# Kernel optimization log

Measured on AMD Instinct MI355X. Metric: run time of the kernel, lower is better.

The kernel has to match this reference:

```python
import jax, jax.numpy as jnp
import numpy as np

N_LAYERS = 4
D = 768
H = 12
DK = D // H
FF = 2048
SD = 5
DIM_LOC = 6
EPS = 1e-10


def layer_norm(x, g, b, eps=1e-5):
    m = x.mean(-1, keepdims=True)
    v = ((x - m) ** 2).mean(-1, keepdims=True)
    return (x - m) / jnp.sqrt(v + eps) * g + b


def calc_pairwise_locs(centers):
    # centers: [b, l, 3] -> [b, l, t, 5] spatial relation features ('center' type, dist-normalized)
    rel = centers[:, :, None, :] - centers[:, None, :, :]
    d = jnp.sqrt(jnp.sum(rel ** 2, -1) + EPS)
    max_d = jnp.max(d.reshape(d.shape[0], -1), -1)
    dn = d / max_d[:, None, None]
    d2 = jnp.sqrt(jnp.sum(rel[..., :2] ** 2, -1) + EPS)
    return jnp.stack([dn, rel[..., 2] / d, d2 / d, rel[..., 1] / d2, rel[..., 0] / d2], -1)


def setup_inputs() -> dict:
    key = jax.random.key(0)
    ks = jax.random.split(key, 32)
    B, L = 16, 512
    std = 0.02
    inp = {
        'obj_embeds': jax.random.normal(ks[0], (B, L, D), jnp.float32),
        'obj_locs': jax.random.uniform(ks[1], (B, L, DIM_LOC), jnp.float32) * 5.0,
        'obj_masks': jnp.ones((B, L), jnp.bool_),
        # single loc layer (obj_loc_encoding='same_all')
        'loc_w': jax.random.normal(ks[2], (DIM_LOC, D), jnp.float32) * std,
        'loc_b': jnp.zeros((D,), jnp.float32),
        'loc_ln_g': jnp.ones((D,), jnp.float32),
        'loc_ln_b': jnp.zeros((D,), jnp.float32),
        # per-layer params, stacked on leading layer dim
        'Wq': jax.random.normal(ks[3], (N_LAYERS, D, D), jnp.float32) * std,
        'bq': jnp.zeros((N_LAYERS, D), jnp.float32),
        'Wk': jax.random.normal(ks[4], (N_LAYERS, D, D), jnp.float32) * std,
        'bk': jnp.zeros((N_LAYERS, D), jnp.float32),
        'Wv': jax.random.normal(ks[5], (N_LAYERS, D, D), jnp.float32) * std,
        'bv': jnp.zeros((N_LAYERS, D), jnp.float32),
        'Wfc': jax.random.normal(ks[6], (N_LAYERS, D, D), jnp.float32) * std,
        'bfc': jnp.zeros((N_LAYERS, D), jnp.float32),
        'loc_fc_w': jax.random.normal(ks[7], (N_LAYERS, SD, H), jnp.float32) * std,
        'loc_fc_b': jnp.zeros((N_LAYERS, H), jnp.float32),
        'ln0_g': jnp.ones((N_LAYERS, D), jnp.float32),
        'ln0_b': jnp.zeros((N_LAYERS, D), jnp.float32),
        'W1': jax.random.normal(ks[8], (N_LAYERS, D, FF), jnp.float32) * std,
        'b1': jnp.zeros((N_LAYERS, FF), jnp.float32),
        'W2': jax.random.normal(ks[9], (N_LAYERS, FF, D), jnp.float32) * std,
        'b2': jnp.zeros((N_LAYERS, D), jnp.float32),
        'ln1_g': jnp.ones((N_LAYERS, D), jnp.float32),
        'ln1_b': jnp.zeros((N_LAYERS, D), jnp.float32),
        'ln2_g': jnp.ones((N_LAYERS, D), jnp.float32),
        'ln2_b': jnp.zeros((N_LAYERS, D), jnp.float32),
    }
    return inp


def _forward(obj_embeds, obj_locs, obj_masks, loc_w, loc_b, loc_ln_g, loc_ln_b,
             Wq, bq, Wk, bk, Wv, bv, Wfc, bfc, loc_fc_w, loc_fc_b, ln0_g, ln0_b,
             W1, b1, W2, b2, ln1_g, ln1_b, ln2_g, ln2_b):
    B, L, _ = obj_embeds.shape
    pl = calc_pairwise_locs(obj_locs[..., :3])        # [b,l,t,5]
    kpm = jnp.logical_not(obj_masks)                  # key_padding_mask: True = pad
    mask = kpm[:, None, None, :]                      # [b,1,1,t]
    query_pos = layer_norm(obj_locs @ loc_w + loc_b, loc_ln_g, loc_ln_b)
    x = obj_embeds
    scale = np.float32(1.0 / np.sqrt(DK))
    for i in range(N_LAYERS):
        x = x + query_pos  # obj_loc_encoding='same_all': add loc embedding every layer
        res = x
        q = (x @ Wq[i] + bq[i]).reshape(B, L, H, DK)
        k = (x @ Wk[i] + bk[i]).reshape(B, L, H, DK)
        v = (x @ Wv[i] + bv[i]).reshape(B, L, H, DK)
        attn = jnp.einsum('blhk,bthk->bhlt', q, k) * scale
        loc_attn = jax.nn.relu(jnp.einsum('bltd,dh->bhlt', pl, loc_fc_w[i])
                               + loc_fc_b[i][None, :, None, None])
        attn = jnp.where(mask, -1e30, attn)
        loc_attn = jnp.where(mask, 0.0, loc_attn)
        fused = jax.nn.softmax(jnp.log(jnp.clip(loc_attn, 1e-6)) + attn, axis=-1)
        out = jnp.einsum('bhlt,bthv->blhv', fused, v).reshape(B, L, D)
        out = out @ Wfc[i] + bfc[i]
        x2 = layer_norm(out + res, ln0_g[i], ln0_b[i])   # attn-internal residual + LN
        x = layer_norm(x + x2, ln1_g[i], ln1_b[i])       # encoder-layer norm1
        ff = jax.nn.gelu(x @ W1[i] + b1[i], approximate=False) @ W2[i] + b2[i]
        x = layer_norm(x + ff, ln2_g[i], ln2_b[i])       # encoder-layer norm2
    return x


def reference(obj_embeds, obj_locs, obj_masks, loc_w, loc_b, loc_ln_g, loc_ln_b,
              Wq, bq, Wk, bk, Wv, bv, Wfc, bfc, loc_fc_w, loc_fc_b, ln0_g, ln0_b,
              W1, b1, W2, b2, ln1_g, ln1_b, ln2_g, ln2_b):
    return _forward(obj_embeds, obj_locs, obj_masks, loc_w, loc_b, loc_ln_g, loc_ln_b,
                    Wq, bq, Wk, bk, Wv, bv, Wfc, bfc, loc_fc_w, loc_fc_b, ln0_g, ln0_b,
                    W1, b1, W2, b2, ln1_g, ln1_b, ln2_g, ln2_b)
```

## Files before the change

### kernel.cpp

```cpp
#include <hip/hip_runtime.h>
#include <hip/hip_bf16.h>
#include <math.h>

#define NL 4
#define D 768
#define H 12
#define DK 64
#define FF 2048
#define SD 5
#define DLOC 6
#define B 16
#define L 512
#define M (B*L)

typedef unsigned short u16;
typedef unsigned int u32;
typedef __attribute__((ext_vector_type(8))) __bf16 bf16x8;
typedef __attribute__((ext_vector_type(4))) float f32x4;

__device__ inline float b2f(u16 u){ u32 v = ((u32)u)<<16; return __builtin_bit_cast(float, v); }
__device__ inline u16 f2b(float f){ __hip_bfloat16 h = __float2bfloat16(f); return __builtin_bit_cast(u16, h); }

__device__ inline void gld16(const u16* g, u16* l) {
    __builtin_amdgcn_global_load_lds(
        (const __attribute__((address_space(1))) u32*)(const void*)g,
        (__attribute__((address_space(3))) u32*)(void*)l, 16, 0, 0);
}

__global__ __launch_bounds__(256) void maxd_kernel(const float* __restrict__ locs,
                                                   u32* __restrict__ maxd) {
    int b = blockIdx.x >> 5;
    int seg = blockIdx.x & 31;
    __shared__ float cx[L], cy[L], cz[L];
    for (int i = threadIdx.x; i < L; i += 256) {
        const float* p = locs + ((size_t)b*L + i)*DLOC;
        cx[i] = p[0]; cy[i] = p[1]; cz[i] = p[2];
    }
    __syncthreads();
    float mx = 0.f;
    int r0 = seg*16;
    #pragma unroll
    for (int r = 0; r < 16; ++r) {
        float px = cx[r0+r], py = cy[r0+r], pz = cz[r0+r];
        for (int c = threadIdx.x; c < L; c += 256) {
            float dx = px-cx[c], dy = py-cy[c], dz = pz-cz[c];
            mx = fmaxf(mx, dx*dx + dy*dy + dz*dz);
        }
    }
    #pragma unroll
    for (int m=1;m<64;m<<=1) mx = fmaxf(mx, __shfl_xor(mx, m));
    __shared__ float wred[4];
    if ((threadIdx.x & 63) == 0) wred[threadIdx.x >> 6] = mx;
    __syncthreads();
    if (threadIdx.x == 0) {
        float v = fmaxf(fmaxf(wred[0],wred[1]), fmaxf(wred[2],wred[3]));
        float d = sqrtf(v + 1e-10f);
        atomicMax(maxd + b, __builtin_bit_cast(u32, d));
    }
}

__global__ __launch_bounds__(256) void initq_kernel(const float* __restrict__ embeds,
    const float* __restrict__ locs, const float* __restrict__ lw, const float* __restrict__ lb,
    const float* __restrict__ lg, const float* __restrict__ lbb,
    float* __restrict__ x, u16* __restrict__ xb) {
    int row = blockIdx.x;
    float lc[DLOC];
    #pragma unroll
    for (int d=0; d<DLOC; d++) lc[d] = locs[(size_t)row*DLOC + d];
    float mv[3], s1 = 0.f, s2 = 0.f;
    #pragma unroll
    for (int e = 0; e < 3; e++) {
        int col = threadIdx.x + 256*e;
        float v = lb[col];
        #pragma unroll
        for (int d = 0; d < DLOC; d++) v += lc[d]*lw[d*D + col];
        mv[e] = v; s1 += v; s2 += v*v;
    }
    __shared__ float r1[256], r2[256];
    r1[threadIdx.x]=s1; r2[threadIdx.x]=s2; __syncthreads();
    for (int s=128;s>0;s>>=1){
        if(threadIdx.x<s){r1[threadIdx.x]+=r1[threadIdx.x+s]; r2[threadIdx.x]+=r2[threadIdx.x+s];}
        __syncthreads();
    }
    float mean = r1[0]*(1.0f/D);
    float var  = r2[0]*(1.0f/D) - mean*mean;
    float rstd = rsqrtf(var + 1e-5f);
    #pragma unroll
    for (int e=0;e<3;e++){
        int col = threadIdx.x+256*e;
        float qp = (mv[e]-mean)*rstd*lg[col]+lbb[col];
        float v = embeds[(size_t)row*D+col] + qp;
        x[(size_t)row*D+col] = v;
        xb[(size_t)row*D+col] = f2b(v);
    }
}

__global__ __launch_bounds__(256) void ln01_kernel(const float* __restrict__ t0f,
    const float* __restrict__ xin,
    const float* __restrict__ g0, const float* __restrict__ b0,
    const float* __restrict__ g1, const float* __restrict__ b1,
    float* __restrict__ xout, u16* __restrict__ xb) {
    int row = blockIdx.x;
    __shared__ float r1[256], r2[256];
    float xv[3], vv[3], s1=0.f, s2=0.f;
    #pragma unroll
    for (int e=0;e<3;e++){
        int col = threadIdx.x+256*e;
        float xr = xin[(size_t)row*D+col];
        float v = t0f[(size_t)row*D+col] + xr;
        xv[e]=xr; vv[e]=v; s1+=v; s2+=v*v;
    }
    r1[threadIdx.x]=s1; r2[threadIdx.x]=s2; __syncthreads();
    for (int s=128;s>0;s>>=1){
        if(threadIdx.x<s){r1[threadIdx.x]+=r1[threadIdx.x+s]; r2[threadIdx.x]+=r2[threadIdx.x+s];}
        __syncthreads();
    }
    float mean0 = r1[0]*(1.0f/D);
    float var0  = r2[0]*(1.0f/D) - mean0*mean0;
    float rstd0 = rsqrtf(var0 + 1e-5f);
    __syncthreads();
    float uv[3]; s1=0.f; s2=0.f;
    #pragma unroll
    for (int e=0;e<3;e++){
        int col = threadIdx.x+256*e;
        float x2 = (vv[e]-mean0)*rstd0*g0[col]+b0[col];
        float u = xv[e] + x2;
        uv[e]=u; s1+=u; s2+=u*u;
    }
    r1[threadIdx.x]=s1; r2[threadIdx.x]=s2; __syncthreads();
    for (int s=128;s>0;s>>=1){
        if(threadIdx.x<s){r1[threadIdx.x]+=r1[threadIdx.x+s]; r2[threadIdx.x]+=r2[threadIdx.x+s];}
        __syncthreads();
    }
    float mean1 = r1[0]*(1.0f/D);
    float var1  = r2[0]*(1.0f/D) - mean1*mean1;
    float rstd1 = rsqrtf(var1 + 1e-5f);
    #pragma unroll
    for (int e=0;e<3;e++){
        int col = threadIdx.x+256*e;
        float v = (uv[e]-mean1)*rstd1*g1[col]+b1[col];
        xout[(size_t)row*D+col] = v;
        xb[(size_t)row*D+col] = f2b(v);
    }
}

template<int LAST>
__global__ __launch_bounds__(256) void ln2q_kernel(const float* __restrict__ xin,
    const float* __restrict__ t0f, const float* __restrict__ g2, const float* __restrict__ b2,
    const float* __restrict__ locs, const float* __restrict__ lw, const float* __restrict__ lb,
    const float* __restrict__ lg, const float* __restrict__ lbb,
    float* __restrict__ xout, u16* __restrict__ xb) {
    int row = blockIdx.x;
    __shared__ float r1[256], r2[256], r3[256], r4[256];
    float lc[DLOC];
    if (!LAST) {
        #pragma unroll
        for (int d=0; d<DLOC; d++) lc[d] = locs[(size_t)row*DLOC + d];
    }
    float vv[3], mv[3], s1=0.f, s2=0.f, s3=0.f, s4=0.f;
    #pragma unroll
    for (int e=0;e<3;e++){
        int col = threadIdx.x+256*e;
        float v = xin[(size_t)row*D+col] + t0f[(size_t)row*D+col];
        vv[e]=v; s1+=v; s2+=v*v;
        if (!LAST) {
            float mvv = lb[col];
            #pragma unroll
            for (int d = 0; d < DLOC; d++) mvv += lc[d]*lw[d*D + col];
            mv[e]=mvv; s3+=mvv; s4+=mvv*mvv;
        }
    }
    r1[threadIdx.x]=s1; r2[threadIdx.x]=s2;
    if (!LAST) { r3[threadIdx.x]=s3; r4[threadIdx.x]=s4; }
    __syncthreads();
    for (int s=128;s>0;s>>=1){
        if(threadIdx.x<s){
            r1[threadIdx.x]+=r1[threadIdx.x+s]; r2[threadIdx.x]+=r2[threadIdx.x+s];
            if (!LAST){ r3[threadIdx.x]+=r3[threadIdx.x+s]; r4[threadIdx.x]+=r4[threadIdx.x+s]; }
        }
        __syncthreads();
    }
    float mean = r1[0]*(1.0f/D);
    float var  = r2[0]*(1.0f/D) - mean*mean;
    float rstd = rsqrtf(var + 1e-5f);
    float mean3=0.f, rstd3=0.f;
    if (!LAST) {
        mean3 = r3[0]*(1.0f/D);
        float var3 = r4[0]*(1.0f/D) - mean3*mean3;
        rstd3 = rsqrtf(var3 + 1e-5f);
    }
    #pragma unroll
    for (int e=0;e<3;e++){
        int col = threadIdx.x+256*e;
        float xn = (vv[e]-mean)*rstd*g2[col]+b2[col];
        if (LAST) {
            xout[(size_t)row*D+col] = xn;
        } else {
            float qp = (mv[e]-mean3)*rstd3*lg[col]+lbb[col];
            float v = xn + qp;
            xout[(size_t)row*D+col] = v;
            xb[(size_t)row*D+col] = f2b(v);
        }
    }
}

__global__ __launch_bounds__(256) void convT6_kernel(
    const float* __restrict__ Wq, const float* __restrict__ Wk,
    const float* __restrict__ Wv, const float* __restrict__ Wfc,
    const float* __restrict__ W1, const float* __restrict__ W2,
    u16* __restrict__ wq_t, u16* __restrict__ wfc_t,
    u16* __restrict__ w1_t, u16* __restrict__ w2_t) {
    int bid = blockIdx.x;
    const float* in; u16* outp; int K, N, nb, kb;
    if (bid < 1728) {
        int m = bid / 576, r = bid % 576;
        in = (m==0) ? Wq : (m==1) ? Wk : Wv;
        outp = wq_t + m*D*D; K = D; N = D; nb = r % 24; kb = r / 24;
    } else if (bid < 2304) {
        int r = bid - 1728;
        in = Wfc; outp = wfc_t; K = D; N = D; nb = r % 24; kb = r / 24;
    } else if (bid < 3840) {
        int r = bid - 2304;
        in = W1; outp = w1_t; K = D; N = FF; nb = r % 64; kb = r / 64;
    } else {
        int r = bid - 3840;
        in = W2; outp = w2_t; K = FF; N = D; nb = r % 24; kb = r / 24;
    }
    __shared__ float tile[32][33];
    int kbb = kb*32, nbb = nb*32;
    int tx = threadIdx.x & 31, ty = threadIdx.x >> 5;
    #pragma unroll
    for (int i=0;i<32;i+=8)
        tile[ty+i][tx] = in[(size_t)(kbb+ty+i)*N + nbb+tx];
    __syncthreads();
    #pragma unroll
    for (int i=0;i<32;i+=8)
        outp[(size_t)(nbb+ty+i)*K + kbb+tx] = f2b(tile[tx][ty+i]);
}

__global__ __launch_bounds__(256) void biaspack_kernel(const float* __restrict__ bq,
    const float* __restrict__ bk, const float* __restrict__ bv, float* __restrict__ outb) {
    int i = blockIdx.x*256 + threadIdx.x;
    int l = i / (3*D), j = i % (3*D);
    float v = (j < D) ? bq[l*D + j] : (j < 2*D ? bk[l*D + j - D] : bv[l*D + j - 2*D]);
    outb[i] = v;
}

template<int OUT_BF16, int ACT>
__global__ __launch_bounds__(256) void mm_kernel(
    const u16* __restrict__ A, const u16* __restrict__ Bt,
    const float* __restrict__ bias, void* __restrict__ Cout, int K, int N)
{
    __shared__ u16 As[2][128*32];
    __shared__ u16 Bs[2][128*32];
    const int tid = threadIdx.x;
    const int lane = tid & 63, wv = tid >> 6;
    const int m0 = blockIdx.y*128, n0 = blockIdx.x*128;
    const int wm = (wv>>1)*64, wn = (wv&1)*64;

    const u16* ag = A  + (size_t)(m0 + wv*16 + (lane>>2))*K + (lane&3)*8;
    const u16* bg = Bt + (size_t)(n0 + wv*16 + (lane>>2))*K + (lane&3)*8;
    const size_t rstep = (size_t)64*K;
    const int lofs = wv*512;

    f32x4 acc[4][4];
    #pragma unroll
    for (int i=0;i<4;i++)
        #pragma unroll
        for (int j=0;j<4;j++) acc[i][j] = (f32x4){0.f,0.f,0.f,0.f};

    const int lr = lane & 15, kq = lane >> 4;

    gld16(ag, &As[0][lofs]);
    gld16(ag + rstep, &As[0][2048+lofs]);
    gld16(bg, &Bs[0][lofs]);
    gld16(bg + rstep, &Bs[0][2048+lofs]);
    __syncthreads();

    int cur = 0;
    for (int k0 = 0; k0 < K; k0 += 32) {
        if (k0 + 32 < K) {
            int nx = cur ^ 1, kn = k0 + 32;
            gld16(ag + kn, &As[nx][lofs]);
            gld16(ag + rstep + kn, &As[nx][2048+lofs]);
            gld16(bg + kn, &Bs[nx][lofs]);
            gld16(bg + rstep + kn, &Bs[nx][2048+lofs]);
        }
        const u16* Arow = &As[cur][(wm + lr)*32 + kq*8];
        const u16* Brow = &Bs[cur][(wn + lr)*32 + kq*8];
        bf16x8 af[4], bfr[4];
        #pragma unroll
        for (int i=0;i<4;i++) af[i]  = *(const bf16x8*)(Arow + i*512);
        #pragma unroll
        for (int j=0;j<4;j++) bfr[j] = *(const bf16x8*)(Brow + j*512);
        #pragma unroll
        for (int i=0;i<4;i++)
            #pragma unroll
            for (int j=0;j<4;j++)
                acc[i][j] = __builtin_amdgcn_mfma_f32_16x16x32_bf16(af[i], bfr[j], acc[i][j], 0,0,0);
        __syncthreads();
        cur ^= 1;
    }

    const int cr = (lane>>4)*4, cc = lane & 15;
    #pragma unroll
    for (int i=0;i<4;i++) {
        int row = m0 + wm + i*16 + cr;
        #pragma unroll
        for (int j=0;j<4;j++) {
            int col = n0 + wn + j*16 + cc;
            float bv_ = bias[col];
            #pragma unroll
            for (int r=0;r<4;r++) {
                float v = acc[i][j][r] + bv_;
                if (ACT) v = 0.5f*v*(1.0f + erff(v*0.70710678f));
                if (OUT_BF16) ((u16*)Cout)[(size_t)(row+r)*N + col] = f2b(v);
                else        ((float*)Cout)[(size_t)(row+r)*N + col] = v;
            }
        }
    }
}

__global__ __launch_bounds__(256) void attn_kernel(
    const u16* __restrict__ qkv, const float* __restrict__ locs,
    const float* __restrict__ maxdp, const float* __restrict__ lfw,
    const float* __restrict__ lfb, u16* __restrict__ out)
{
    const int RS = 3*D;
    const float SC = 0.18033688f;
    const int bid = blockIdx.x;
    const int qt = bid & 7;
    const int hp = (bid >> 3) % 6;
    const int b  = bid / 48;
    const int qb = qt*64;
    const int h0 = hp*2;

    __shared__ u16 Ks[2][64*64];
    __shared__ u16 Vt[2][64*64];
    __shared__ u16 Pl[2][4*16*64];
    __shared__ float Cts[64][4];

    const int t = threadIdx.x;
    const int lane = t & 63, wv = t >> 6;
    const int l15 = lane & 15, l4 = lane >> 4;

    bf16x8 qf[2][2];
    {
        const u16* qr = qkv + (size_t)(b*L + qb + wv*16 + l15)*RS + h0*DK + l4*8;
        qf[0][0] = *(const bf16x8*)(qr);
        qf[0][1] = *(const bf16x8*)(qr + 32);
        qf[1][0] = *(const bf16x8*)(qr + DK);
        qf[1][1] = *(const bf16x8*)(qr + DK + 32);
    }
    float cqx[4], cqy[4], cqz[4];
    #pragma unroll
    for (int r=0;r<4;r++){
        const float* p = locs + (size_t)(b*L + qb + wv*16 + l4*4 + r)*DLOC;
        cqx[r]=p[0]; cqy[r]=p[1]; cqz[r]=p[2];
    }
    const float invmd = 1.0f / maxdp[b];
    float w0p[2], w1[2], w2[2], w3[2], w4[2], wbb[2];
    #pragma unroll
    for (int hh=0; hh<2; hh++){
        int h = h0+hh;
        w0p[hh] = lfw[0*H+h]*invmd; w1[hh]=lfw[1*H+h]; w2[hh]=lfw[2*H+h];
        w3[hh]=lfw[3*H+h]; w4[hh]=lfw[4*H+h]; wbb[hh]=lfb[h];
    }

    f32x4 oacc[2][4];
    float mrun[2][4], lrun[2][4];
    #pragma unroll
    for (int hh=0;hh<2;hh++)
        #pragma unroll
        for (int j=0;j<4;j++){ oacc[hh][j] = (f32x4){0.f,0.f,0.f,0.f};
                               mrun[hh][j] = -1e30f; lrun[hh][j] = 0.f; }

    const int r0s = (wv*64 + lane) >> 3;
    const int sslot = lane & 7;

    bf16x8 kreg[4];
    bf16x8 vreg[2][2];
    float ctr0=0.f, ctr1=0.f, ctr2=0.f;

    {
        const u16* kgb = qkv + (size_t)(b*L + 0)*RS + D + h0*DK;
        kreg[0] = *(const bf16x8*)(kgb + (size_t)r0s*RS + sslot*8);
        kreg[1] = *(const bf16x8*)(kgb + (size_t)(r0s+32)*RS + sslot*8);
        kreg[2] = *(const bf16x8*)(kgb + DK + (size_t)r0s*RS + sslot*8);
        kreg[3] = *(const bf16x8*)(kgb + DK + (size_t)(r0s+32)*RS + sslot*8);
        const u16* vp = qkv + (size_t)(b*L + 0 + lane)*RS + 2*D + h0*DK + wv*16;
        vreg[0][0] = *(const bf16x8*)(vp);
        vreg[0][1] = *(const bf16x8*)(vp + 8);
        vreg[1][0] = *(const bf16x8*)(vp + DK);
        vreg[1][1] = *(const bf16x8*)(vp + DK + 8);
        if (t < 64) {
            const float* p = locs + (size_t)(b*L + 0 + t)*DLOC;
            ctr0=p[0]; ctr1=p[1]; ctr2=p[2];
        }
    }

    for (int kt = 0; kt < L; kt += 64) {
        {
            int c0 = (sslot ^ (r0s & 7))*8;
            *(bf16x8*)(&Ks[0][r0s*64 + c0]) = kreg[0];
            *(bf16x8*)(&Ks[0][(r0s+32)*64 + c0]) = kreg[1];
            *(bf16x8*)(&Ks[1][r0s*64 + c0]) = kreg[2];
            *(bf16x8*)(&Ks[1][(r0s+32)*64 + c0]) = kreg[3];
            int d0 = wv*16;
            #pragma unroll
            for (int hh=0; hh<2; hh++)
                #pragma unroll
                for (int e=0;e<8;e++){
                    Vt[hh][(d0+e)*64   + (lane ^ (e<<3))] = ((const u16*)&vreg[hh][0])[e];
                    Vt[hh][(d0+8+e)*64 + (lane ^ (e<<3))] = ((const u16*)&vreg[hh][1])[e];
                }
            if (t < 64) { Cts[t][0]=ctr0; Cts[t][1]=ctr1; Cts[t][2]=ctr2; }
        }
        __syncthreads();

        if (kt + 64 < L) {
            const u16* kgb = qkv + (size_t)(b*L + kt + 64)*RS + D + h0*DK;
            kreg[0] = *(const bf16x8*)(kgb + (size_t)r0s*RS + sslot*8);
            kreg[1] = *(const bf16x8*)(kgb + (size_t)(r0s+32)*RS + sslot*8);
            kreg[2] = *(const bf16x8*)(kgb + DK + (size_t)r0s*RS + sslot*8);
            kreg[3] = *(const bf16x8*)(kgb + DK + (size_t)(r0s+32)*RS + sslot*8);
            const u16* vp = qkv + (size_t)(b*L + kt + 64 + lane)*RS + 2*D + h0*DK + wv*16;
            vreg[0][0] = *(const bf16x8*)(vp);
            vreg[0][1] = *(const bf16x8*)(vp + 8);
            vreg[1][0] = *(const bf16x8*)(vp + DK);
            vreg[1][1] = *(const bf16x8*)(vp + DK + 8);
            if (t < 64) {
                const float* p = locs + (size_t)(b*L + kt + 64 + t)*DLOC;
                ctr0=p[0]; ctr1=p[1]; ctr2=p[2];
            }
        }

        f32x4 sacc[2][4];
        #pragma unroll
        for (int hh=0;hh<2;hh++)
            #pragma unroll
            for (int j=0;j<4;j++){
                sacc[hh][j] = (f32x4){0.f,0.f,0.f,0.f};
                #pragma unroll
                for (int c=0;c<2;c++){
                    int row = j*16 + l15;
                    int slot = l4 + 4*c;
                    bf16x8 kf = *(const bf16x8*)(&Ks[hh][row*64 + ((slot ^ (row&7))*8)]);
                    sacc[hh][j] = __builtin_amdgcn_mfma_f32_16x16x32_bf16(qf[hh][c], kf, sacc[hh][j], 0,0,0);
                }
            }

        float ctx[4], cty[4], ctz[4];
        #pragma unroll
        for (int j=0;j<4;j++){
            int c = l15 + 16*j;
            ctx[j]=Cts[c][0]; cty[j]=Cts[c][1]; ctz[j]=Cts[c][2];
        }

        float alr[2][4];
        #pragma unroll
        for (int r=0;r<4;r++){
            float f0[4], f1[4], f2[4], f3[4], f4[4];
            #pragma unroll
            for (int j=0;j<4;j++){
                float rx = cqx[r]-ctx[j], ry = cqy[r]-cty[j], rz = cqz[r]-ctz[j];
                float d2e = fmaf(ry,ry, fmaf(rx,rx, 1e-10f));
                float r2  = fmaf(rz,rz, d2e);
                float invd  = __builtin_amdgcn_rsqf(r2);
                float invd2 = __builtin_amdgcn_rsqf(d2e);
                f0[j] = r2*invd;
                f1[j] = rz*invd;
                f2[j] = (d2e*invd2)*invd;
                f3[j] = ry*invd2;
                f4[j] = rx*invd2;
            }
            #pragma unroll
            for (int hh=0; hh<2; hh++){
                float sv[4], la[4];
                #pragma unroll
                for (int j=0;j<4;j++){
                    float z = fmaf(f0[j], w0p[hh],
                              fmaf(f1[j], w1[hh],
                              fmaf(f2[j], w2[hh],
                              fmaf(f3[j], w3[hh],
                              fmaf(f4[j], w4[hh], wbb[hh])))));
                    la[j] = fmaxf(z, 1e-6f);
                    sv[j] = sacc[hh][j][r]*SC;
                }
                float mx = fmaxf(fmaxf(sv[0],sv[1]), fmaxf(sv[2],sv[3]));
                #pragma unroll
                for (int msk=1; msk<16; msk<<=1) mx = fmaxf(mx, __shfl_xor(mx, msk));
                float mo = mrun[hh][r];
                float mn = fmaxf(mo, mx);
                float al = __builtin_amdgcn_exp2f(mo - mn);
                float sp = 0.f;
                u16* pw = &Pl[hh][wv*1024];
                int q = l4*4 + r, sw = (q&7)<<3;
                #pragma unroll
                for (int j=0;j<4;j++){
                    float p = la[j] * __builtin_amdgcn_exp2f(sv[j] - mn);
                    sp += p;
                    pw[q*64 + ((l15 + 16*j) ^ sw)] = f2b(p);
                }
                #pragma unroll
                for (int msk=1; msk<16; msk<<=1) sp += __shfl_xor(sp, msk);
                mrun[hh][r] = mn;
                lrun[hh][r] = lrun[hh][r]*al + sp;
                alr[hh][r] = al;
            }
        }

        #pragma unroll
        for (int hh=0; hh<2; hh++){
            #pragma unroll
            for (int j=0;j<4;j++)
                #pragma unroll
                for (int r=0;r<4;r++) oacc[hh][j][r] *= alr[hh][r];
            const u16* pr = &Pl[hh][wv*1024];
            #pragma unroll
            for (int c=0;c<2;c++){
                int prow = l15;
                int pslot = l4 + 4*c;
                bf16x8 pf = *(const bf16x8*)(pr + prow*64 + ((pslot ^ (prow&7))*8));
                #pragma unroll
                for (int j=0;j<4;j++){
                    int vrow = j*16 + l15;
                    int vslot = l4 + 4*c;
                    bf16x8 vf = *(const bf16x8*)(&Vt[hh][vrow*64 + ((vslot ^ (vrow&7))*8)]);
                    oacc[hh][j] = __builtin_amdgcn_mfma_f32_16x16x32_bf16(pf, vf, oacc[hh][j], 0,0,0);
                }
            }
        }
        __syncthreads();
    }

    #pragma unroll
    for (int hh=0; hh<2; hh++)
        #pragma unroll
        for (int r=0;r<4;r++){
            float inv = __builtin_amdgcn_rcpf(lrun[hh][r]);
            size_t obase = (size_t)(b*L + qb + wv*16 + l4*4 + r)*D + (h0+hh)*DK;
            #pragma unroll
            for (int j=0;j<4;j++)
                out[obase + l15 + 16*j] = f2b(oacc[hh][j][r] * inv);
        }
}

extern "C" void kernel_launch(void* const* d_in, const int* in_sizes, int n_in,
                              void* d_out, int out_size, void* d_ws, size_t ws_size,
                              hipStream_t stream) {
    const float* obj_embeds = (const float*)d_in[0];
    const float* obj_locs   = (const float*)d_in[1];
    const float* loc_w   = (const float*)d_in[3];
    const float* loc_b   = (const float*)d_in[4];
    const float* loc_ln_g= (const float*)d_in[5];
    const float* loc_ln_b= (const float*)d_in[6];
    const float* Wq = (const float*)d_in[7];
    const float* bq = (const float*)d_in[8];
    const float* Wk = (const float*)d_in[9];
    const float* bk = (const float*)d_in[10];
    const float* Wv = (const float*)d_in[11];
    const float* bv = (const float*)d_in[12];
    const float* Wfc= (const float*)d_in[13];
    const float* bfc= (const float*)d_in[14];
    const float* lfw= (const float*)d_in[15];
    const float* lfb= (const float*)d_in[16];
    const float* ln0_g = (const float*)d_in[17];
    const float* ln0_b = (const float*)d_in[18];
    const float* W1 = (const float*)d_in[19];
    const float* b1 = (const float*)d_in[20];
    const float* W2 = (const float*)d_in[21];
    const float* b2 = (const float*)d_in[22];
    const float* ln1_g = (const float*)d_in[23];
    const float* ln1_b = (const float*)d_in[24];
    const float* ln2_g = (const float*)d_in[25];
    const float* ln2_b = (const float*)d_in[26];

    float* x  = (float*)d_out;
    char* base = (char*)d_ws;
    u16*   xb    = (u16*)  (base);
    u16*   qkv   = (u16*)  (base + 12582912);
    u16*   aob   = (u16*)  (base + 50331648);
    float* t0f   = (float*)(base + 62914560);
    u16*   wq_t  = (u16*)  (base + 88080384);
    u16*   wfc_t = (u16*)  (base + 91619328);
    u16*   w1_t  = (u16*)  (base + 92798976);
    u16*   w2_t  = (u16*)  (base + 95944704);
    float* bqkv  = (float*)(base + 99090432);
    u32*   maxd  = (u32*)  (base + 99127296);
    u16*   h1b   = qkv;

    hipMemsetAsync(maxd, 0, B*sizeof(u32), stream);
    maxd_kernel<<<B*32, 256, 0, stream>>>(obj_locs, maxd);
    biaspack_kernel<<<(NL*3*D)/256, 256, 0, stream>>>(bq, bk, bv, bqkv);
    initq_kernel<<<M, 256, 0, stream>>>(obj_embeds, obj_locs, loc_w, loc_b,
                                        loc_ln_g, loc_ln_b, x, xb);

    for (int i = 0; i < NL; i++) {
        const size_t wo = (size_t)i*D*D;
        convT6_kernel<<<5376, 256, 0, stream>>>(Wq + wo, Wk + wo, Wv + wo, Wfc + wo,
                                                W1 + (size_t)i*D*FF, W2 + (size_t)i*FF*D,
                                                wq_t, wfc_t, w1_t, w2_t);

        mm_kernel<1,0><<<dim3(18,64), 256, 0, stream>>>(xb, wq_t, bqkv + i*3*D, qkv, D, 3*D);
        attn_kernel<<<B*6*8, 256, 0, stream>>>(qkv, obj_locs, (const float*)maxd,
                                               lfw + i*SD*H, lfb + i*H, aob);
        mm_kernel<0,0><<<dim3(6,64), 256, 0, stream>>>(aob, wfc_t, bfc + i*D, t0f, D, D);
        ln01_kernel<<<M, 256, 0, stream>>>(t0f, x, ln0_g + i*D, ln0_b + i*D,
                                           ln1_g + i*D, ln1_b + i*D, x, xb);
        mm_kernel<1,1><<<dim3(16,64), 256, 0, stream>>>(xb, w1_t, b1 + i*FF, h1b, D, FF);
        mm_kernel<0,0><<<dim3(6,64), 256, 0, stream>>>(h1b, w2_t, b2 + i*D, t0f, FF, D);
        if (i < NL-1)
            ln2q_kernel<0><<<M, 256, 0, stream>>>(x, t0f, ln2_g + i*D, ln2_b + i*D,
                obj_locs, loc_w, loc_b, loc_ln_g, loc_ln_b, x, xb);
        else
            ln2q_kernel<1><<<M, 256, 0, stream>>>(x, t0f, ln2_g + i*D, ln2_b + i*D,
                obj_locs, loc_w, loc_b, loc_ln_g, loc_ln_b, x, xb);
    }
}
```

Measured before the change: 1.353 ms.

## Cut attention kernel registers and LDS to raise occupancy

The attention kernel now targets four blocks per SIMD through launch bounds. It shrinks LDS by letting the P tile share the K buffer after an extra barrier. K tiles are loaded straight into LDS with global_load_lds rather than staged through registers, and Q is reloaded each iteration instead of kept live. Register prefetching of the next K/V tile is dropped, so latency hiding relies on having more resident waves, at the cost of an extra sync per tile and repeated Q loads.

```diff
diff --git a/kernel.cpp b/kernel.cpp
--- a/kernel.cpp
+++ b/kernel.cpp
@@ -321,7 +321,7 @@
     }
 }
 
-__global__ __launch_bounds__(256) void attn_kernel(
+__global__ __launch_bounds__(256, 4) void attn_kernel(
     const u16* __restrict__ qkv, const float* __restrict__ locs,
     const float* __restrict__ maxdp, const float* __restrict__ lfw,
     const float* __restrict__ lfb, u16* __restrict__ out)
@@ -335,23 +335,14 @@
     const int qb = qt*64;
     const int h0 = hp*2;
 
-    __shared__ u16 Ks[2][64*64];
-    __shared__ u16 Vt[2][64*64];
-    __shared__ u16 Pl[2][4*16*64];
+    __shared__ u16 KP[2][4096];
+    __shared__ u16 Vt[2][4096];
     __shared__ float Cts[64][4];
 
     const int t = threadIdx.x;
     const int lane = t & 63, wv = t >> 6;
     const int l15 = lane & 15, l4 = lane >> 4;
 
-    bf16x8 qf[2][2];
-    {
-        const u16* qr = qkv + (size_t)(b*L + qb + wv*16 + l15)*RS + h0*DK + l4*8;
-        qf[0][0] = *(const bf16x8*)(qr);
-        qf[0][1] = *(const bf16x8*)(qr + 32);
-        qf[1][0] = *(const bf16x8*)(qr + DK);
-        qf[1][1] = *(const bf16x8*)(qr + DK + 32);
-    }
     float cqx[4], cqy[4], cqz[4];
     #pragma unroll
     for (int r=0;r<4;r++){
@@ -376,90 +367,66 @@
                                mrun[hh][j] = -1e30f; lrun[hh][j] = 0.f; }
 
     const int r0s = (wv*64 + lane) >> 3;
-    const int sslot = lane & 7;
-
-    bf16x8 kreg[4];
-    bf16x8 vreg[2][2];
-    float ctr0=0.f, ctr1=0.f, ctr2=0.f;
-
-    {
-        const u16* kgb = qkv + (size_t)(b*L + 0)*RS + D + h0*DK;
-        kreg[0] = *(const bf16x8*)(kgb + (size_t)r0s*RS + sslot*8);
-        kreg[1] = *(const bf16x8*)(kgb + (size_t)(r0s+32)*RS + sslot*8);
-        kreg[2] = *(const bf16x8*)(kgb + DK + (size_t)r0s*RS + sslot*8);
-        kreg[3] = *(const bf16x8*)(kgb + DK + (size_t)(r0s+32)*RS + sslot*8);
-        const u16* vp = qkv + (size_t)(b*L + 0 + lane)*RS + 2*D + h0*DK + wv*16;
-        vreg[0][0] = *(const bf16x8*)(vp);
-        vreg[0][1] = *(const bf16x8*)(vp + 8);
-        vreg[1][0] = *(const bf16x8*)(vp + DK);
-        vreg[1][1] = *(const bf16x8*)(vp + DK + 8);
+    const int c0 = ((lane & 7) ^ (r0s & 7))*8;
+    const u16* qr = qkv + (size_t)(b*L + qb + wv*16 + l15)*RS + h0*DK + l4*8;
+
+    for (int kt = 0; kt < L; kt += 64) {
+        const u16* kgb = qkv + (size_t)(b*L + kt)*RS + D + h0*DK;
+        gld16(kgb + (size_t)r0s*RS + c0,           &KP[0][wv*512]);
+        gld16(kgb + (size_t)(r0s+32)*RS + c0,      &KP[0][2048 + wv*512]);
+        gld16(kgb + DK + (size_t)r0s*RS + c0,      &KP[1][wv*512]);
+        gld16(kgb + DK + (size_t)(r0s+32)*RS + c0, &KP[1][2048 + wv*512]);
+        const u16* vp = qkv + (size_t)(b*L + kt + lane)*RS + 2*D + h0*DK + wv*16;
+        bf16x8 v0a = *(const bf16x8*)(vp);
+        bf16x8 v0b = *(const bf16x8*)(vp + 8);
+        bf16x8 v1a = *(const bf16x8*)(vp + DK);
+        bf16x8 v1b = *(const bf16x8*)(vp + DK + 8);
+        bf16x8 qf00 = *(const bf16x8*)(qr);
+        bf16x8 qf01 = *(const bf16x8*)(qr + 32);
+        bf16x8 qf10 = *(const bf16x8*)(qr + DK);
+        bf16x8 qf11 = *(const bf16x8*)(qr + DK + 32);
         if (t < 64) {
-            const float* p = locs + (size_t)(b*L + 0 + t)*DLOC;
-            ctr0=p[0]; ctr1=p[1]; ctr2=p[2];
-        }
-    }
-
-    for (int kt = 0; kt < L; kt += 64) {
+            const float* p = locs + (size_t)(b*L + kt + t)*DLOC;
+            Cts[t][0]=p[0]; Cts[t][1]=p[1]; Cts[t][2]=p[2];
+        }
+        __syncthreads();
+
         {
-            int c0 = (sslot ^ (r0s & 7))*8;
-            *(bf16x8*)(&Ks[0][r0s*64 + c0]) = kreg[0];
-            *(bf16x8*)(&Ks[0][(r0s+32)*64 + c0]) = kreg[1];
-            *(bf16x8*)(&Ks[1][r0s*64 + c0]) = kreg[2];
-            *(bf16x8*)(&Ks[1][(r0s+32)*64 + c0]) = kreg[3];
             int d0 = wv*16;
             #pragma unroll
-            for (int hh=0; hh<2; hh++)
-                #pragma unroll
-                for (int e=0;e<8;e++){
-                    Vt[hh][(d0+e)*64   + (lane ^ (e<<3))] = ((const u16*)&vreg[hh][0])[e];
-                    Vt[hh][(d0+8+e)*64 + (lane ^ (e<<3))] = ((const u16*)&vreg[hh][1])[e];
-                }
-            if (t < 64) { Cts[t][0]=ctr0; Cts[t][1]=ctr1; Cts[t][2]=ctr2; }
-        }
-        __syncthreads();
-
-        if (kt + 64 < L) {
-            const u16* kgb = qkv + (size_t)(b*L + kt + 64)*RS + D + h0*DK;
-            kreg[0] = *(const bf16x8*)(kgb + (size_t)r0s*RS + sslot*8);
-            kreg[1] = *(const bf16x8*)(kgb + (size_t)(r0s+32)*RS + sslot*8);
-            kreg[2] = *(const bf16x8*)(kgb + DK + (size_t)r0s*RS + sslot*8);
-            kreg[3] = *(const bf16x8*)(kgb + DK + (size_t)(r0s+32)*RS + sslot*8);
-            const u16* vp = qkv + (size_t)(b*L + kt + 64 + lane)*RS + 2*D + h0*DK + wv*16;
-            vreg[0][0] = *(const bf16x8*)(vp);
-            vreg[0][1] = *(const bf16x8*)(vp + 8);
-            vreg[1][0] = *(const bf16x8*)(vp + DK);
-            vreg[1][1] = *(const bf16x8*)(vp + DK + 8);
-            if (t < 64) {
-                const float* p = locs + (size_t)(b*L + kt + 64 + t)*DLOC;
-                ctr0=p[0]; ctr1=p[1]; ctr2=p[2];
-            }
-        }
-
+            for (int e=0;e<8;e++){
+                int csw = lane ^ (e<<3);
+                Vt[0][(d0+e)*64   + csw] = ((const u16*)&v0a)[e];
+                Vt[0][(d0+8+e)*64 + csw] = ((const u16*)&v0b)[e];
+                Vt[1][(d0+e)*64   + csw] = ((const u16*)&v1a)[e];
+                Vt[1][(d0+8+e)*64 + csw] = ((const u16*)&v1b)[e];
+            }
+        }
         f32x4 sacc[2][4];
         #pragma unroll
-        for (int hh=0;hh<2;hh++)
+        for (int j=0;j<4;j++){
+            int row = j*16 + l15;
+            sacc[0][j] = (f32x4){0.f,0.f,0.f,0.f};
+            sacc[1][j] = (f32x4){0.f,0.f,0.f,0.f};
+            #pragma unroll
+            for (int c=0;c<2;c++){
+                int ofs = row*64 + (((l4 + 4*c) ^ (row&7))*8);
+                bf16x8 kf0 = *(const bf16x8*)(&KP[0][ofs]);
+                bf16x8 kf1 = *(const bf16x8*)(&KP[1][ofs]);
+                sacc[0][j] = __builtin_amdgcn_mfma_f32_16x16x32_bf16(c?qf01:qf00, kf0, sacc[0][j], 0,0,0);
+                sacc[1][j] = __builtin_amdgcn_mfma_f32_16x16x32_bf16(c?qf11:qf10, kf1, sacc[1][j], 0,0,0);
+            }
+        }
+        __syncthreads();
+
+        #pragma unroll
+        for (int r=0;r<4;r++){
+            float ctx[4], cty[4], ctz[4];
             #pragma unroll
             for (int j=0;j<4;j++){
-                sacc[hh][j] = (f32x4){0.f,0.f,0.f,0.f};
-                #pragma unroll
-                for (int c=0;c<2;c++){
-                    int row = j*16 + l15;
-                    int slot = l4 + 4*c;
-                    bf16x8 kf = *(const bf16x8*)(&Ks[hh][row*64 + ((slot ^ (row&7))*8)]);
-                    sacc[hh][j] = __builtin_amdgcn_mfma_f32_16x16x32_bf16(qf[hh][c], kf, sacc[hh][j], 0,0,0);
-                }
-            }
-
-        float ctx[4], cty[4], ctz[4];
-        #pragma unroll
-        for (int j=0;j<4;j++){
-            int c = l15 + 16*j;
-            ctx[j]=Cts[c][0]; cty[j]=Cts[c][1]; ctz[j]=Cts[c][2];
-        }
-
-        float alr[2][4];
-        #pragma unroll
-        for (int r=0;r<4;r++){
+                int c = l15 + 16*j;
+                ctx[j]=Cts[c][0]; cty[j]=Cts[c][1]; ctz[j]=Cts[c][2];
+            }
             float f0[4], f1[4], f2[4], f3[4], f4[4];
             #pragma unroll
             for (int j=0;j<4;j++){
@@ -494,7 +461,7 @@
                 float mn = fmaxf(mo, mx);
                 float al = __builtin_amdgcn_exp2f(mo - mn);
                 float sp = 0.f;
-                u16* pw = &Pl[hh][wv*1024];
+                u16* pw = &KP[hh][wv*1024];
                 int q = l4*4 + r, sw = (q&7)<<3;
                 #pragma unroll
                 for (int j=0;j<4;j++){
@@ -506,27 +473,22 @@
                 for (int msk=1; msk<16; msk<<=1) sp += __shfl_xor(sp, msk);
                 mrun[hh][r] = mn;
                 lrun[hh][r] = lrun[hh][r]*al + sp;
-                alr[hh][r] = al;
+                #pragma unroll
+                for (int j=0;j<4;j++) oacc[hh][j][r] *= al;
             }
         }
 
         #pragma unroll
         for (int hh=0; hh<2; hh++){
-            #pragma unroll
-            for (int j=0;j<4;j++)
-                #pragma unroll
-                for (int r=0;r<4;r++) oacc[hh][j][r] *= alr[hh][r];
-            const u16* pr = &Pl[hh][wv*1024];
+            const u16* pr = &KP[hh][wv*1024];
             #pragma unroll
             for (int c=0;c<2;c++){
-                int prow = l15;
-                int pslot = l4 + 4*c;
-                bf16x8 pf = *(const bf16x8*)(pr + prow*64 + ((pslot ^ (prow&7))*8));
+                int pofs = l15*64 + (((l4 + 4*c) ^ (l15&7))*8);
+                bf16x8 pf = *(const bf16x8*)(pr + pofs);
                 #pragma unroll
                 for (int j=0;j<4;j++){
                     int vrow = j*16 + l15;
-                    int vslot = l4 + 4*c;
-                    bf16x8 vf = *(const bf16x8*)(&Vt[hh][vrow*64 + ((vslot ^ (vrow&7))*8)]);
+                    bf16x8 vf = *(const bf16x8*)(&Vt[hh][vrow*64 + (((l4 + 4*c) ^ (vrow&7))*8)]);
                     oacc[hh][j] = __builtin_amdgcn_mfma_f32_16x16x32_bf16(pf, vf, oacc[hh][j], 0,0,0);
                 }
             }
```

Measured after the change: 1.608 ms. +18.8%, slower.
